# Kernel optimization log

Measured on AMD Instinct MI355X. Metric: run time of the kernel, lower is better.

Reference implementation:

```python
import jax, jax.numpy as jnp
import numpy as np

DCR = 8      # depth_channel_ratio
CLIP = 0.3   # clipping_ratio
ITER = 32    # iterative_num
EPS = 1e-6


def setup_inputs() -> dict:
    key = jax.random.key(0)
    k1, k2 = jax.random.split(key)
    B, C, H, W = 8, 128, 96, 320
    input_features = jax.random.normal(k1, (B, C, H, W), dtype=jnp.float32)
    dynamic_masks = jax.random.randint(k2, (B, H, W), 0, 2, dtype=jnp.int32)
    return {"input_features": input_features, "dynamic_masks": dynamic_masks}


def _channel_selection(x):
    # Select 2*(C//DCR) channels most similar to pseudo disparity/depth ramps.
    B, C, H, W = x.shape
    disp = jnp.linspace(0.1, 1.0, H, dtype=x.dtype)                      # (H,)
    disp_full = jnp.broadcast_to(disp[None, :, None], (B, H, W)).reshape(-1)  # (B*H*W,)
    depth_full = 1.0 - disp_full
    s = jax.nn.sigmoid(x).transpose(1, 0, 2, 3).reshape(C, -1)           # (C, B*H*W)
    sn = jnp.maximum(jnp.sqrt(jnp.sum(s * s, axis=-1)), EPS)             # (C,)

    def cos_sim(v):
        vn = jnp.maximum(jnp.sqrt(jnp.sum(v * v)), EPS)
        return (s @ v) / (sn * vn)                                       # (C,)

    nsel = C // DCR
    disp_idx = jnp.argsort(-cos_sim(disp_full))[:nsel]
    depth_idx = jnp.argsort(-cos_sim(depth_full))[:nsel]
    return jnp.concatenate([disp_idx, depth_idx])                        # (2*nsel,)


def _clip_norm(v, clip_ratio):
    # per-(batch,channel) max over spatial dims, scaled, zero->1, clamp to [0,1]
    m = jnp.max(v, axis=(2, 3), keepdims=True) * clip_ratio
    m = jnp.where(m == 0, jnp.ones_like(m), m)
    return jnp.clip(v / m, 0.0, 1.0)


def reference(input_features, dynamic_masks):
    B, C, H, W = input_features.shape
    idx = _channel_selection(input_features)
    sel = input_features[:, idx]                       # (B, ns, H, W)
    # mask resolution == feature resolution, so nearest resize is identity
    m = dynamic_masks.astype(input_features.dtype)[:, None]  # (B,1,H,W) broadcast over ns
    iters = int(ITER * H / dynamic_masks.shape[1])     # == ITER here (static)

    pad_bottom = lambda t: jnp.concatenate([t, t[:, :, -1:]], axis=2)
    prop0 = pad_bottom(sel)                            # (B, ns, H+1, W)

    def step(prop, _):
        core = m * prop[:, :, 1:] + (1.0 - m) * sel    # pull values up one row where masked
        return pad_bottom(core), None

    prop, _ = jax.lax.scan(step, prop0, None, length=iters)
    prop = prop[:, :, :-1]                             # (B, ns, H, W)

    w = _clip_norm(jnp.abs(prop - sel), CLIP)
    w = jnp.max(w, axis=1, keepdims=True)              # (B,1,H,W)
    refined = w * prop + (1.0 - w) * sel
    return input_features.at[:, idx].set(refined)
```

## Files before the change

kernel.cpp:

```cpp
#include <hip/hip_runtime.h>
#include <cstdint>
#include <cstddef>

#define BB 8
#define CC 128
#define HH 96
#define WW 320
#define HW (HH*WW)
#define NSEL 32
#define NSELH 16
#define U1 6

__device__ __forceinline__ float sigmoidf_(float x) {
  return __builtin_amdgcn_rcpf(1.0f + __expf(-x));
}

__global__ __launch_bounds__(256) void k_copy_reduce(
    const float* __restrict__ x, float* __restrict__ out,
    double* __restrict__ partials) {
  int bc = blockIdx.x;
  const float4* __restrict__ xi = (const float4*)(x + (size_t)bc * HW);
  float4* __restrict__ oi = (float4*)(out + (size_t)bc * HW);
  int t = threadIdx.x;
  float tf = 0.0f, af = 0.0f, qf = 0.0f;
  for (int base = 0; base < HW/4; base += 256*U1) {
    float4 v[U1];
    #pragma unroll
    for (int u = 0; u < U1; u++) v[u] = xi[base + u*256 + t];
    #pragma unroll
    for (int u = 0; u < U1; u++) {
      int j = base + u*256 + t;
      oi[j] = v[u];
      int h = j / (WW/4);
      float d = 0.1f + (float)h * (0.9f/95.0f);
      float s0 = sigmoidf_(v[u].x), s1 = sigmoidf_(v[u].y);
      float s2 = sigmoidf_(v[u].z), s3 = sigmoidf_(v[u].w);
      float ts = (s0+s1)+(s2+s3);
      tf += ts;
      af += ts * d;
      qf += (s0*s0+s1*s1)+(s2*s2+s3*s3);
    }
  }
  __shared__ double sh[3][256];
  sh[0][t]=(double)tf; sh[1][t]=(double)af; sh[2][t]=(double)qf;
  __syncthreads();
  for (int ofs=128; ofs>0; ofs>>=1) {
    if (t < ofs) {
      sh[0][t]+=sh[0][t+ofs];
      sh[1][t]+=sh[1][t+ofs];
      sh[2][t]+=sh[2][t+ofs];
    }
    __syncthreads();
  }
  if (t==0) {
    partials[bc*3+0]=sh[0][0];
    partials[bc*3+1]=sh[1][0];
    partials[bc*3+2]=sh[2][0];
  }
}

__global__ __launch_bounds__(CC) void k_select(
    const double* __restrict__ partials, int* __restrict__ idx) {
  int c = threadIdx.x;
  double T=0.0, A=0.0, Q=0.0;
  for (int b=0;b<BB;b++) {
    int bc = b*CC + c;
    T += partials[bc*3+0];
    A += partials[bc*3+1];
    Q += partials[bc*3+2];
  }
  double sn = sqrt(Q); if (sn < 1e-6) sn = 1e-6;
  double c1 = A / sn;
  double c2 = (T - A) / sn;
  __shared__ double s1[CC], s2[CC];
  s1[c]=c1; s2[c]=c2;
  __syncthreads();
  int r1=0, r2=0;
  for (int j=0;j<CC;j++) {
    r1 += (s1[j] > c1) || (s1[j]==c1 && j<c);
    r2 += (s2[j] > c2) || (s2[j]==c2 && j<c);
  }
  if (r1 < NSELH) idx[r1] = c;
  if (r2 < NSELH) idx[NSELH + r2] = c;
}

__global__ __launch_bounds__(64) void k_runs(
    const int* __restrict__ mask, uint8_t* __restrict__ kk) {
  int b = blockIdx.x / 5;
  int w = (blockIdx.x % 5)*64 + threadIdx.x;
  const int* __restrict__ mcol = mask + (size_t)b*HW + w;
  unsigned long long lo=0ull, hi=0ull;
  #pragma unroll
  for (int h=0; h<64; ++h) lo |= (unsigned long long)(mcol[h*WW]!=0) << h;
  #pragma unroll
  for (int h=64; h<95; ++h) hi |= (unsigned long long)(mcol[h*WW]!=0) << (h-64);
  uint8_t* __restrict__ kcol = kk + (size_t)b*HW + w;
  #pragma unroll
  for (int h=0; h<96; ++h) {
    unsigned long long s;
    if (h == 0)      s = lo;
    else if (h < 64) s = (lo >> h) | (hi << (64-h));
    else             s = hi >> (h-64);
    int run = __builtin_ctzll(~s | (1ull<<33));
    kcol[h*WW] = (uint8_t)(run > 32 ? 32 : run);
  }
}

__global__ __launch_bounds__(256) void k_maxdiff(
    const float* __restrict__ x, const int* __restrict__ idx,
    const uint8_t* __restrict__ kk, float* __restrict__ mclip) {
  int b = blockIdx.x >> 5;
  int c = blockIdx.x & 31;
  int ic = idx[c];
  const float* __restrict__ base = x + ((size_t)b*CC + ic)*HW;
  const uint8_t* __restrict__ kb = kk + (size_t)b*HW;
  float mx = 0.0f;
  for (int j = threadIdx.x; j < HW/4; j += 256) {
    float4 sel = ((const float4*)base)[j];
    uchar4 kv  = ((const uchar4*)kb)[j];
    int h = j / (WW/4);
    int w4 = (j - h*(WW/4))*4;
    float p0 = base[(h+(int)kv.x)*WW + w4+0];
    float p1 = base[(h+(int)kv.y)*WW + w4+1];
    float p2 = base[(h+(int)kv.z)*WW + w4+2];
    float p3 = base[(h+(int)kv.w)*WW + w4+3];
    mx = fmaxf(mx, fmaxf(fmaxf(fabsf(p0-sel.x), fabsf(p1-sel.y)),
                         fmaxf(fabsf(p2-sel.z), fabsf(p3-sel.w))));
  }
  __shared__ float sh[256];
  sh[threadIdx.x]=mx; __syncthreads();
  for (int ofs=128; ofs>0; ofs>>=1) {
    if ((int)threadIdx.x<ofs) sh[threadIdx.x]=fmaxf(sh[threadIdx.x], sh[threadIdx.x+ofs]);
    __syncthreads();
  }
  if (threadIdx.x==0) {
    float m = sh[0] * 0.3f;
    if (m == 0.0f) m = 1.0f;
    mclip[blockIdx.x] = m;
  }
}

__global__ __launch_bounds__(WW) void k_refine(
    const float* __restrict__ x, const int* __restrict__ idx,
    const uint8_t* __restrict__ kk, const float* __restrict__ mclip,
    float* __restrict__ out) {
  int bh = blockIdx.x;
  int b = bh / HH, h = bh - b*HH;
  int w = threadIdx.x;
  __shared__ int sidx[NSEL];
  __shared__ float smc[NSEL];
  if (threadIdx.x < NSEL) {
    sidx[threadIdx.x] = idx[threadIdx.x];
    smc[threadIdx.x]  = mclip[b*NSEL + threadIdx.x];
  }
  __syncthreads();
  int r = h + (int)kk[(size_t)bh*WW + w];
  float sel[NSEL], prop[NSEL];
  float wmax = 0.0f;
  #pragma unroll
  for (int c=0;c<NSEL;c++) {
    const float* __restrict__ base = x + ((size_t)b*CC + sidx[c])*HW;
    sel[c]  = base[h*WW + w];
    prop[c] = base[r*WW + w];
    float v = fabsf(prop[c]-sel[c]) / smc[c];
    wmax = fmaxf(wmax, fminf(v, 1.0f));
  }
  #pragma unroll
  for (int c=0;c<NSEL;c++) {
    float rf = wmax*prop[c] + (1.0f - wmax)*sel[c];
    out[((size_t)b*CC + sidx[c])*HW + h*WW + w] = rf;
  }
}

extern "C" void kernel_launch(void* const* d_in, const int* in_sizes, int n_in,
                              void* d_out, int out_size, void* d_ws, size_t ws_size,
                              hipStream_t stream) {
  const float* x   = (const float*)d_in[0];
  const int* mask  = (const int*)d_in[1];
  float* out       = (float*)d_out;

  char* ws = (char*)d_ws;
  double* partials = (double*)(ws);
  int*    idx      = (int*)(ws + 24576);
  float*  mclip    = (float*)(ws + 24576 + 128);
  uint8_t* kk      = (uint8_t*)(ws + 24576 + 128 + 1024);

  k_copy_reduce<<<BB*CC, 256, 0, stream>>>(x, out, partials);
  k_select<<<1, CC, 0, stream>>>(partials, idx);
  k_runs<<<BB*5, 64, 0, stream>>>(mask, kk);
  k_maxdiff<<<BB*NSEL, 256, 0, stream>>>(x, idx, kk, mclip);
  k_refine<<<BB*HH, WW, 0, stream>>>(x, idx, kk, mclip, out);
}
```

Before: 103.4 us.

## Fuse max-diff computation into copy/reduce pass for all channels

Runs the mask run-length kernel first, then folds the per-(batch,channel) propagated max-abs-difference into the copy/sigmoid reduction kernel for every channel, so the separate maxdiff pass over the selected channels goes away. The select kernel now picks the clip maxima for the chosen channels. This trades a second read of the 32 selected channels for extra gather loads and max work across all 128 channels. It also reorders the unrolled loop with a sched barrier and iterates the outer loop in reverse.

```diff
diff --git a/kernel.cpp b/kernel.cpp
--- a/kernel.cpp
+++ b/kernel.cpp
@@ -9,79 +9,12 @@
 #define HW (HH*WW)
 #define NSEL 32
 #define NSELH 16
-#define U1 6
+#define OUTERS 6
+
+typedef float f32x4 __attribute__((ext_vector_type(4)));
 
 __device__ __forceinline__ float sigmoidf_(float x) {
   return __builtin_amdgcn_rcpf(1.0f + __expf(-x));
-}
-
-__global__ __launch_bounds__(256) void k_copy_reduce(
-    const float* __restrict__ x, float* __restrict__ out,
-    double* __restrict__ partials) {
-  int bc = blockIdx.x;
-  const float4* __restrict__ xi = (const float4*)(x + (size_t)bc * HW);
-  float4* __restrict__ oi = (float4*)(out + (size_t)bc * HW);
-  int t = threadIdx.x;
-  float tf = 0.0f, af = 0.0f, qf = 0.0f;
-  for (int base = 0; base < HW/4; base += 256*U1) {
-    float4 v[U1];
-    #pragma unroll
-    for (int u = 0; u < U1; u++) v[u] = xi[base + u*256 + t];
-    #pragma unroll
-    for (int u = 0; u < U1; u++) {
-      int j = base + u*256 + t;
-      oi[j] = v[u];
-      int h = j / (WW/4);
-      float d = 0.1f + (float)h * (0.9f/95.0f);
-      float s0 = sigmoidf_(v[u].x), s1 = sigmoidf_(v[u].y);
-      float s2 = sigmoidf_(v[u].z), s3 = sigmoidf_(v[u].w);
-      float ts = (s0+s1)+(s2+s3);
-      tf += ts;
-      af += ts * d;
-      qf += (s0*s0+s1*s1)+(s2*s2+s3*s3);
-    }
-  }
-  __shared__ double sh[3][256];
-  sh[0][t]=(double)tf; sh[1][t]=(double)af; sh[2][t]=(double)qf;
-  __syncthreads();
-  for (int ofs=128; ofs>0; ofs>>=1) {
-    if (t < ofs) {
-      sh[0][t]+=sh[0][t+ofs];
-      sh[1][t]+=sh[1][t+ofs];
-      sh[2][t]+=sh[2][t+ofs];
-    }
-    __syncthreads();
-  }
-  if (t==0) {
-    partials[bc*3+0]=sh[0][0];
-    partials[bc*3+1]=sh[1][0];
-    partials[bc*3+2]=sh[2][0];
-  }
-}
-
-__global__ __launch_bounds__(CC) void k_select(
-    const double* __restrict__ partials, int* __restrict__ idx) {
-  int c = threadIdx.x;
-  double T=0.0, A=0.0, Q=0.0;
-  for (int b=0;b<BB;b++) {
-    int bc = b*CC + c;
-    T += partials[bc*3+0];
-    A += partials[bc*3+1];
-    Q += partials[bc*3+2];
-  }
-  double sn = sqrt(Q); if (sn < 1e-6) sn = 1e-6;
-  double c1 = A / sn;
-  double c2 = (T - A) / sn;
-  __shared__ double s1[CC], s2[CC];
-  s1[c]=c1; s2[c]=c2;
-  __syncthreads();
-  int r1=0, r2=0;
-  for (int j=0;j<CC;j++) {
-    r1 += (s1[j] > c1) || (s1[j]==c1 && j<c);
-    r2 += (s2[j] > c2) || (s2[j]==c2 && j<c);
-  }
-  if (r1 < NSELH) idx[r1] = c;
-  if (r2 < NSELH) idx[NSELH + r2] = c;
 }
 
 __global__ __launch_bounds__(64) void k_runs(
@@ -106,43 +39,110 @@
   }
 }
 
-__global__ __launch_bounds__(256) void k_maxdiff(
-    const float* __restrict__ x, const int* __restrict__ idx,
-    const uint8_t* __restrict__ kk, float* __restrict__ mclip) {
-  int b = blockIdx.x >> 5;
-  int c = blockIdx.x & 31;
-  int ic = idx[c];
-  const float* __restrict__ base = x + ((size_t)b*CC + ic)*HW;
+__global__ __launch_bounds__(256) void k_copy_reduce_max(
+    const float* __restrict__ x, float* __restrict__ out,
+    const uint8_t* __restrict__ kk,
+    double* __restrict__ partials, float* __restrict__ pmax) {
+  int t = threadIdx.x;
+  int bc = blockIdx.x;
+  int b = bc >> 7;
+  const float* __restrict__ xp = x + (size_t)bc * HW;
+  const f32x4* __restrict__ xi = (const f32x4*)xp;
+  f32x4* __restrict__ oi = (f32x4*)(out + (size_t)bc * HW);
   const uint8_t* __restrict__ kb = kk + (size_t)b*HW;
-  float mx = 0.0f;
-  for (int j = threadIdx.x; j < HW/4; j += 256) {
-    float4 sel = ((const float4*)base)[j];
-    uchar4 kv  = ((const uchar4*)kb)[j];
-    int h = j / (WW/4);
-    int w4 = (j - h*(WW/4))*4;
-    float p0 = base[(h+(int)kv.x)*WW + w4+0];
-    float p1 = base[(h+(int)kv.y)*WW + w4+1];
-    float p2 = base[(h+(int)kv.z)*WW + w4+2];
-    float p3 = base[(h+(int)kv.w)*WW + w4+3];
-    mx = fmaxf(mx, fmaxf(fmaxf(fabsf(p0-sel.x), fabsf(p1-sel.y)),
-                         fmaxf(fabsf(p2-sel.z), fabsf(p3-sel.w))));
+  float tf = 0.f, af = 0.f, qf = 0.f, mxf = 0.f;
+  #pragma unroll 1
+  for (int o = OUTERS-1; o >= 0; --o) {
+    int base = o*1280;
+    f32x4 v[5]; unsigned kv[5];
+    #pragma unroll
+    for (int u = 0; u < 5; ++u) {
+      int j = base + u*256 + t;
+      v[u] = xi[j];
+      int h = j / 80, w4 = (j - h*80)*4;
+      kv[u] = *(const unsigned*)(kb + h*WW + w4);
+    }
+    __builtin_amdgcn_sched_barrier(0);
+    #pragma unroll
+    for (int u = 0; u < 5; ++u) oi[base + u*256 + t] = v[u];
+    #pragma unroll
+    for (int u = 0; u < 5; ++u) {
+      int j = base + u*256 + t;
+      int h = j / 80, w4 = (j - h*80)*4;
+      unsigned k4 = kv[u];
+      float p0 = xp[(h + (int)(k4       & 0xffu))*WW + w4 + 0];
+      float p1 = xp[(h + (int)((k4>>8)  & 0xffu))*WW + w4 + 1];
+      float p2 = xp[(h + (int)((k4>>16) & 0xffu))*WW + w4 + 2];
+      float p3 = xp[(h + (int)( k4>>24        ))*WW + w4 + 3];
+      mxf = fmaxf(mxf, fmaxf(fmaxf(fabsf(p0-v[u].x), fabsf(p1-v[u].y)),
+                             fmaxf(fabsf(p2-v[u].z), fabsf(p3-v[u].w))));
+      float d = 0.1f + (float)h * (0.9f/95.0f);
+      float s0 = sigmoidf_(v[u].x), s1 = sigmoidf_(v[u].y);
+      float s2 = sigmoidf_(v[u].z), s3 = sigmoidf_(v[u].w);
+      float ts = (s0+s1)+(s2+s3);
+      tf += ts;
+      af += ts * d;
+      qf += (s0*s0+s1*s1)+(s2*s2+s3*s3);
+    }
   }
-  __shared__ float sh[256];
-  sh[threadIdx.x]=mx; __syncthreads();
+  __shared__ double sh[3][256];
+  __shared__ float shm[256];
+  sh[0][t]=(double)tf; sh[1][t]=(double)af; sh[2][t]=(double)qf; shm[t]=mxf;
+  __syncthreads();
   for (int ofs=128; ofs>0; ofs>>=1) {
-    if ((int)threadIdx.x<ofs) sh[threadIdx.x]=fmaxf(sh[threadIdx.x], sh[threadIdx.x+ofs]);
+    if (t < ofs) {
+      sh[0][t]+=sh[0][t+ofs];
+      sh[1][t]+=sh[1][t+ofs];
+      sh[2][t]+=sh[2][t+ofs];
+      shm[t] = fmaxf(shm[t], shm[t+ofs]);
+    }
     __syncthreads();
   }
-  if (threadIdx.x==0) {
-    float m = sh[0] * 0.3f;
-    if (m == 0.0f) m = 1.0f;
-    mclip[blockIdx.x] = m;
+  if (t==0) {
+    partials[bc*3+0]=sh[0][0];
+    partials[bc*3+1]=sh[1][0];
+    partials[bc*3+2]=sh[2][0];
+    pmax[bc]=shm[0];
   }
+}
+
+__global__ __launch_bounds__(CC) void k_select(
+    const double* __restrict__ partials, const float* __restrict__ pmax,
+    int* __restrict__ idx, float* __restrict__ smc) {
+  int c = threadIdx.x;
+  double T=0.0, A=0.0, Q=0.0;
+  for (int b=0;b<BB;b++) {
+    int p = b*CC + c;
+    T += partials[p*3+0];
+    A += partials[p*3+1];
+    Q += partials[p*3+2];
+  }
+  double sn = sqrt(Q); if (sn < 1e-6) sn = 1e-6;
+  double c1 = A / sn;
+  double c2 = (T - A) / sn;
+  __shared__ double s1[CC], s2[CC];
+  s1[c]=c1; s2[c]=c2;
+  __syncthreads();
+  int r1=0, r2=0;
+  for (int j=0;j<CC;j++) {
+    r1 += (s1[j] > c1) || (s1[j]==c1 && j<c);
+    r2 += (s2[j] > c2) || (s2[j]==c2 && j<c);
+  }
+  if (r1 < NSELH || r2 < NSELH) {
+    for (int b=0;b<BB;b++) {
+      float m = pmax[b*CC + c] * 0.3f;
+      if (m == 0.0f) m = 1.0f;
+      if (r1 < NSELH) smc[b*NSEL + r1] = m;
+      if (r2 < NSELH) smc[b*NSEL + NSELH + r2] = m;
+    }
+  }
+  if (r1 < NSELH) idx[r1] = c;
+  if (r2 < NSELH) idx[NSELH + r2] = c;
 }
 
 __global__ __launch_bounds__(WW) void k_refine(
     const float* __restrict__ x, const int* __restrict__ idx,
-    const uint8_t* __restrict__ kk, const float* __restrict__ mclip,
+    const uint8_t* __restrict__ kk, const float* __restrict__ smcin,
     float* __restrict__ out) {
   int bh = blockIdx.x;
   int b = bh / HH, h = bh - b*HH;
@@ -151,7 +151,7 @@
   __shared__ float smc[NSEL];
   if (threadIdx.x < NSEL) {
     sidx[threadIdx.x] = idx[threadIdx.x];
-    smc[threadIdx.x]  = mclip[b*NSEL + threadIdx.x];
+    smc[threadIdx.x]  = smcin[b*NSEL + threadIdx.x];
   }
   __syncthreads();
   int r = h + (int)kk[(size_t)bh*WW + w];
@@ -181,13 +181,13 @@
 
   char* ws = (char*)d_ws;
   double* partials = (double*)(ws);
-  int*    idx      = (int*)(ws + 24576);
-  float*  mclip    = (float*)(ws + 24576 + 128);
-  uint8_t* kk      = (uint8_t*)(ws + 24576 + 128 + 1024);
+  float*  pmax     = (float*)(ws + 24576);
+  int*    idx      = (int*)(ws + 24576 + 4096);
+  float*  smc      = (float*)(ws + 24576 + 4096 + 128);
+  uint8_t* kk      = (uint8_t*)(ws + 24576 + 4096 + 128 + 1024);
 
-  k_copy_reduce<<<BB*CC, 256, 0, stream>>>(x, out, partials);
-  k_select<<<1, CC, 0, stream>>>(partials, idx);
   k_runs<<<BB*5, 64, 0, stream>>>(mask, kk);
-  k_maxdiff<<<BB*NSEL, 256, 0, stream>>>(x, idx, kk, mclip);
-  k_refine<<<BB*HH, WW, 0, stream>>>(x, idx, kk, mclip, out);
+  k_copy_reduce_max<<<BB*CC, 256, 0, stream>>>(x, out, kk, partials, pmax);
+  k_select<<<1, CC, 0, stream>>>(partials, pmax, idx, smc);
+  k_refine<<<BB*HH, WW, 0, stream>>>(x, idx, kk, smc, out);
 }
```

After: 104.9 us. No clear change (+1.4%).
